# Kernel optimization log

Hardware: AMD Instinct MI355X
Metric: run time of the kernel (lower is better)

Reference implementation:

```python
import jax, jax.numpy as jnp
from jax import lax
import numpy as np

B, L, C = 16, 4096, 512
G = 8            # n_groups
CG = C // G      # group_dim = 64
WD = 4           # weather_dim
ORF = 10.0       # offset_range_factor


def conv1d(x, w, b=None):
    # x: [N, Cin, L], w: [Cout, Cin, 3], stride 1, padding 1
    y = lax.conv_general_dilated(x, w, window_strides=(1,), padding=[(1, 1)],
                                 dimension_numbers=('NCH', 'OIH', 'NCH'))
    if b is not None:
        y = y + b[None, :, None]
    return y


def group_norm(x, gamma, beta, groups=4, eps=1e-5):
    N, Cc, Ln = x.shape
    xr = x.reshape(N, groups, Cc // groups, Ln)
    mu = xr.mean(axis=(2, 3), keepdims=True)
    var = ((xr - mu) ** 2).mean(axis=(2, 3), keepdims=True)
    xn = ((xr - mu) / jnp.sqrt(var + eps)).reshape(N, Cc, Ln)
    return xn * gamma[None, :, None] + beta[None, :, None]


def grid_sample_bilinear_border(inp, grid):
    # Faithful torch F.grid_sample(mode='bilinear', padding_mode='border', align_corners=True)
    # inp: [N, C, H, W]; grid: [N, Ho, Wo, 2], grid[...,0]=x (width coord), grid[...,1]=y (height coord)
    N, Cc, H, W = inp.shape
    _, Ho, Wo, _ = grid.shape
    gx, gy = grid[..., 0], grid[..., 1]
    ix = jnp.clip((gx + 1.0) * 0.5 * (W - 1), 0.0, W - 1)  # border padding clamps coords
    iy = jnp.clip((gy + 1.0) * 0.5 * (H - 1), 0.0, H - 1)
    ix0f = jnp.floor(ix); iy0f = jnp.floor(iy)
    wx = ix - ix0f; wy = iy - iy0f
    ix0 = jnp.clip(ix0f.astype(jnp.int32), 0, W - 1)
    iy0 = jnp.clip(iy0f.astype(jnp.int32), 0, H - 1)
    ix1 = jnp.clip(ix0 + 1, 0, W - 1)
    iy1 = jnp.clip(iy0 + 1, 0, H - 1)
    flat = inp.reshape(N, Cc, H * W)
    def gather(iyk, ixk):
        idx = (iyk * W + ixk).reshape(N, 1, Ho * Wo)
        return jnp.take_along_axis(flat, idx, axis=2).reshape(N, Cc, Ho, Wo)
    v00 = gather(iy0, ix0); v01 = gather(iy0, ix1)
    v10 = gather(iy1, ix0); v11 = gather(iy1, ix1)
    wx = wx[:, None, :, :]; wy = wy[:, None, :, :]
    return (v00 * (1 - wy) * (1 - wx) + v01 * (1 - wy) * wx
            + v10 * wy * (1 - wx) + v11 * wy * wx)


def _forward(x, x_ext, w1, b1, gn_g, gn_b, w2, b2, w3, gate):
    xt = jnp.transpose(x, (0, 2, 1))              # [B, C, L]
    xg = xt.reshape(B * G, CG, L)                 # [B*G, CG, L]
    xe = jnp.transpose(x_ext, (0, 2, 1))          # [B, WD, L]
    xe = jnp.tile(xe, (G, 1, 1))                  # torch .repeat(n_groups,1,1)
    pin = jnp.concatenate([xg, xe], axis=1)       # [B*G, CG+WD, L]
    h = jax.nn.gelu(group_norm(conv1d(pin, w1, b1), gn_g, gn_b), approximate=False)
    h = jax.nn.gelu(conv1d(h, w2, b2), approximate=False)
    offset = jnp.tanh(conv1d(h, w3)) * ORF        # [B*G, 1, L]
    off_n = offset * (2.0 / (L - 1.0))
    ref = (jnp.linspace(0.5, L - 0.5, L, dtype=x.dtype) / (L - 1.0)) * 2.0 - 1.0
    grid_x = jnp.clip(ref[None, None, :, None] + off_n[..., None], -1.0, 1.0)  # [B*G,1,L,1]
    grid = jnp.concatenate([grid_x, jnp.zeros_like(grid_x)], axis=-1)
    grid = jnp.transpose(grid, (0, 2, 1, 3))      # [B*G, L, 1, 2]
    xs = grid_sample_bilinear_border(xg[..., None], grid)[..., 0]  # [B*G, CG, L]
    x_out = xg + jnp.tanh(gate) * xs
    x_out = x_out.reshape(B, C, L)
    return jnp.transpose(x_out, (0, 2, 1)), offset


def setup_inputs() -> dict:
    key = jax.random.key(0)
    ks = jax.random.split(key, 8)
    s = 0.05
    return {
        'x': jax.random.normal(ks[0], (B, L, C), jnp.float32),
        'x_ext': jax.random.normal(ks[1], (B, L, WD), jnp.float32),
        'w1': jax.random.normal(ks[2], (64, CG + WD, 3), jnp.float32) * s,
        'b1': jax.random.normal(ks[3], (64,), jnp.float32) * s,
        'gn_g': jnp.ones((64,), jnp.float32),
        'gn_b': jnp.zeros((64,), jnp.float32),
        'w2': jax.random.normal(ks[4], (32, 64, 3), jnp.float32) * s,
        'b2': jax.random.normal(ks[5], (32,), jnp.float32) * s,
        'w3': jax.random.normal(ks[6], (1, 32, 3), jnp.float32) * s,
        'gate': jnp.array([0.5], jnp.float32),
    }


def reference(x, x_ext, w1, b1, gn_g, gn_b, w2, b2, w3, gate):
    return _forward(x, x_ext, w1, b1, gn_g, gn_b, w2, b2, w3, gate)
```

## Files before the change

### kernel.cpp

```cpp
#include <hip/hip_runtime.h>
#include <hip/hip_bf16.h>

#define BB 16
#define LL 4096
#define CC 512
#define NG 128
#define IC1 68
#define OC1 64
#define OC2 32

typedef short short8 __attribute__((ext_vector_type(8)));
typedef float f32x4 __attribute__((ext_vector_type(4)));

__device__ inline ushort f2b(float f) {
    __hip_bfloat16 h = __float2bfloat16(f);
    return *reinterpret_cast<ushort*>(&h);
}
__device__ inline float b2f(ushort u) {
    __hip_bfloat16 h;
    *reinterpret_cast<ushort*>(&h) = u;
    return __bfloat162float(h);
}
__device__ inline float fast_tanh(float y) {
    float e = __expf(2.0f * y);
    return 1.0f - 2.0f / (e + 1.0f);
}
__device__ inline float fast_gelu(float x) {
    float y = x * (0.7978845608f + 0.0356774081f * x * x);
    return 0.5f * x * (1.0f + fast_tanh(y));
}

__global__ __launch_bounds__(256) void k_prep(const float* __restrict__ x,
    const float* __restrict__ w1, const float* __restrict__ w2,
    const float* __restrict__ gate,
    ushort* __restrict__ w1b, ushort* __restrict__ w2b, float* __restrict__ corr)
{
    int idx = blockIdx.x * 256 + threadIdx.x;
    if (idx < 18432) {
        int k = idx / 6144; int r = idx - k * 6144;
        int oc = r / 96;    int icp = r - oc * 96;
        float v = (icp < IC1) ? w1[(oc * IC1 + icp) * 3 + k] : 0.0f;
        w1b[idx] = f2b(v);
    } else if (idx < 24576) {
        int j = idx - 18432;
        int k = j / 2048; int r = j - k * 2048;
        int oc = r / 64;  int ic = r - oc * 64;
        w2b[j] = f2b(w2[(oc * OC1 + ic) * 3 + k]);
    } else if (idx < 32768) {
        int i3 = idx - 24576;
        int b = i3 >> 9; int ch = i3 & 511;
        float tg = tanhf(gate[0]);
        corr[i3] = tg * 0.5f *
            (x[((size_t)(b * LL + 2047)) * CC + ch] +
             x[((size_t)(b * LL + 2048)) * CC + ch]);
    }
}

#define K1_ROWS 130
#define K1_STR  104
__global__ __launch_bounds__(256) void ka_stats(const float* __restrict__ x,
    const float* __restrict__ xe, const float* __restrict__ b1,
    const ushort* __restrict__ w1b, float* __restrict__ part)
{
    __shared__ ushort pin[K1_ROWS * K1_STR];
    const int n = blockIdx.y, lt = blockIdx.x;
    const int b = n >> 3, g = n & 7, be = n & 15;
    const int l0 = lt * 128;
    const int t = threadIdx.x;

    {
        const int q = t & 15;
        for (int pos = t; pos < K1_ROWS * 16; pos += 256) {
            int li = pos >> 4;
            int l = l0 - 1 + li;
            float4 v = make_float4(0.f, 0.f, 0.f, 0.f);
            if (l >= 0 && l < LL)
                v = *(const float4*)&x[((size_t)(b * LL + l)) * CC + g * 64 + q * 4];
            uint lo = (uint)f2b(v.x) | ((uint)f2b(v.y) << 16);
            uint hi = (uint)f2b(v.z) | ((uint)f2b(v.w) << 16);
            *(uint2*)&pin[li * K1_STR + q * 4] = make_uint2(lo, hi);
        }
    }
    for (int li = t; li < K1_ROWS; li += 256) {
        int l = l0 - 1 + li;
        float4 v = make_float4(0.f, 0.f, 0.f, 0.f);
        if (l >= 0 && l < LL)
            v = *(const float4*)&xe[(size_t)(be * LL + l) * 4];
        uint lo = (uint)f2b(v.x) | ((uint)f2b(v.y) << 16);
        uint hi = (uint)f2b(v.z) | ((uint)f2b(v.w) << 16);
        *(uint2*)&pin[li * K1_STR + 64] = make_uint2(lo, hi);
    }
    {
        uint* pz = (uint*)pin;
        for (int pos = t; pos < K1_ROWS * 14; pos += 256) {
            int li = pos / 14, j = pos - li * 14;
            pz[li * 52 + 34 + j] = 0u;
        }
    }
    __syncthreads();

    const int lane = t & 63;
    const int w = t >> 6;
    const int och = w & 1, lh = w >> 1;
    const int m = lane & 15, h = lane >> 4;

    short8 fa[2][9];
#pragma unroll
    for (int mi = 0; mi < 2; ++mi)
#pragma unroll
        for (int k = 0; k < 3; ++k)
#pragma unroll
            for (int c = 0; c < 3; ++c)
                fa[mi][k * 3 + c] = *(const short8*)&w1b[
                    (size_t)(k * 64 + och * 32 + mi * 16 + m) * 96 + c * 32 + h * 8];

    f32x4 acc[2][4] = {};
#pragma unroll
    for (int tt = 0; tt < 4; ++tt) {
        const int rowbase = lh * 64 + tt * 16 + m;
#pragma unroll
        for (int k = 0; k < 3; ++k) {
#pragma unroll
            for (int c = 0; c < 3; ++c) {
                short8 fb = *(const short8*)&pin[(rowbase + k) * K1_STR + c * 32 + h * 8];
                acc[0][tt] = __builtin_amdgcn_mfma_f32_16x16x32_bf16(fa[0][k * 3 + c], fb, acc[0][tt], 0, 0, 0);
                acc[1][tt] = __builtin_amdgcn_mfma_f32_16x16x32_bf16(fa[1][k * 3 + c], fb, acc[1][tt], 0, 0, 0);
            }
        }
    }

#pragma unroll
    for (int mi = 0; mi < 2; ++mi) {
        float bias[4];
#pragma unroll
        for (int r = 0; r < 4; ++r)
            bias[r] = b1[och * 32 + mi * 16 + h * 4 + r];
        float s1 = 0.f, s2 = 0.f;
#pragma unroll
        for (int tt = 0; tt < 4; ++tt) {
            float v0 = acc[mi][tt][0] + bias[0];
            float v1 = acc[mi][tt][1] + bias[1];
            float v2 = acc[mi][tt][2] + bias[2];
            float v3 = acc[mi][tt][3] + bias[3];
            s1 += v0 + v1 + v2 + v3;
            s2 += v0 * v0 + v1 * v1 + v2 * v2 + v3 * v3;
        }
#pragma unroll
        for (int off = 32; off > 0; off >>= 1) {
            s1 += __shfl_down(s1, off, 64);
            s2 += __shfl_down(s2, off, 64);
        }
        if (lane == 0) {
            int gidx = och * 2 + mi;
            part[(((size_t)n * 4 + gidx) * 64 + lt * 2 + lh) * 2 + 0] = s1;
            part[(((size_t)n * 4 + gidx) * 64 + lt * 2 + lh) * 2 + 1] = s2;
        }
    }
}

#define BT 124
#define XR 130
#define P2R 130
#define P2STR 72
#define H2STR 132
__global__ __launch_bounds__(256) void kb_fused(const float* __restrict__ x,
    const float* __restrict__ xe, const float* __restrict__ b1,
    const ushort* __restrict__ w1b, const float* __restrict__ part,
    const float* __restrict__ gn_g, const float* __restrict__ gn_b,
    const float* __restrict__ b2, const ushort* __restrict__ w2b,
    const float* __restrict__ w3, const float* __restrict__ corr,
    float* __restrict__ out, float* __restrict__ offs)
{
    __shared__ ushort pin[XR * K1_STR];
    __shared__ ushort p2[P2R * P2STR];
    __shared__ float sstats[8];
    const int n = blockIdx.y, lt = blockIdx.x;
    const int b = n >> 3, g = n & 7, be = n & 15;
    const int l0 = lt * BT;
    const int t = threadIdx.x;
    const int lane = t & 63;
    const int w = t >> 6;

    {
        float2 p = *(const float2*)&part[(((size_t)n * 4 + w) * 64 + lane) * 2];
        float s1 = p.x, s2 = p.y;
#pragma unroll
        for (int off = 32; off > 0; off >>= 1) {
            s1 += __shfl_down(s1, off, 64);
            s2 += __shfl_down(s2, off, 64);
        }
        if (lane == 0) {
            float mean = s1 * (1.0f / 65536.0f);
            float var  = s2 * (1.0f / 65536.0f) - mean * mean;
            sstats[w * 2 + 0] = mean;
            sstats[w * 2 + 1] = 1.0f / sqrtf(var + 1e-5f);
        }
    }

    {
        const int q = t & 15;
        const float4 corrv = *(const float4*)&corr[(b << 9) + g * 64 + q * 4];
        for (int pos = t; pos < XR * 16; pos += 256) {
            int li = pos >> 4;
            int l = l0 - 3 + li;
            float4 v = make_float4(0.f, 0.f, 0.f, 0.f);
            if (l >= 0 && l < LL) {
                v = *(const float4*)&x[((size_t)(b * LL + l)) * CC + g * 64 + q * 4];
                if (li >= 3 && li < 3 + BT) {
                    float4 o;
                    o.x = v.x + corrv.x; o.y = v.y + corrv.y;
                    o.z = v.z + corrv.z; o.w = v.w + corrv.w;
                    *(float4*)&out[((size_t)(b * LL + l)) * CC + g * 64 + q * 4] = o;
                }
            }
            uint lo = (uint)f2b(v.x) | ((uint)f2b(v.y) << 16);
            uint hi = (uint)f2b(v.z) | ((uint)f2b(v.w) << 16);
            *(uint2*)&pin[li * K1_STR + q * 4] = make_uint2(lo, hi);
        }
        for (int li = t; li < XR; li += 256) {
            int l = l0 - 3 + li;
            float4 v = make_float4(0.f, 0.f, 0.f, 0.f);
            if (l >= 0 && l < LL)
                v = *(const float4*)&xe[(size_t)(be * LL + l) * 4];
            uint lo = (uint)f2b(v.x) | ((uint)f2b(v.y) << 16);
            uint hi = (uint)f2b(v.z) | ((uint)f2b(v.w) << 16);
            *(uint2*)&pin[li * K1_STR + 64] = make_uint2(lo, hi);
        }
        uint* pz = (uint*)pin;
        for (int pos = t; pos < XR * 14; pos += 256) {
            int li = pos / 14, j = pos - li * 14;
            pz[li * 52 + 34 + j] = 0u;
        }
        uint* qz = (uint*)p2;
        for (int i = t; i < 72; i += 256)
            qz[128 * 36 + i] = 0u;
    }
    __syncthreads();

    const int och = w & 1, lh = w >> 1;
    const int m = lane & 15, h = lane >> 4;

    short8 fa[2][9];
#pragma unroll
    for (int mi = 0; mi < 2; ++mi)
#pragma unroll
        for (int k = 0; k < 3; ++k)
#pragma unroll
            for (int c = 0; c < 3; ++c)
                fa[mi][k * 3 + c] = *(const short8*)&w1b[
                    (size_t)(k * 64 + och * 32 + mi * 16 + m) * 96 + c * 32 + h * 8];

    f32x4 acc[2][4] = {};
#pragma unroll
    for (int tt = 0; tt < 4; ++tt) {
        const int rowbase = lh * 64 + tt * 16 + m;
#pragma unroll
        for (int k = 0; k < 3; ++k) {
#pragma unroll
            for (int c = 0; c < 3; ++c) {
                short8 fb = *(const short8*)&pin[(rowbase + k) * K1_STR + c * 32 + h * 8];
                acc[0][tt] = __builtin_amdgcn_mfma_f32_16x16x32_bf16(fa[0][k * 3 + c], fb, acc[0][tt], 0, 0, 0);
                acc[1][tt] = __builtin_amdgcn_mfma_f32_16x16x32_bf16(fa[1][k * 3 + c], fb, acc[1][tt], 0, 0, 0);
            }
        }
    }

#pragma unroll
    for (int mi = 0; mi < 2; ++mi) {
        int gi = och * 2 + mi;
        float mean = sstats[gi * 2], istd = sstats[gi * 2 + 1];
        float A_[4], B_[4];
#pragma unroll
        for (int r = 0; r < 4; ++r) {
            int oc = och * 32 + mi * 16 + h * 4 + r;
            float ga = gn_g[oc];
            A_[r] = istd * ga;
            B_[r] = gn_b[oc] + (b1[oc] - mean) * A_[r];
        }
#pragma unroll
        for (int tt = 0; tt < 4; ++tt) {
            int p = lh * 64 + tt * 16 + m;
            int l = l0 - 2 + p;
            uint2 pk = make_uint2(0u, 0u);
            if (l >= 0 && l < LL) {
                float v0 = fast_gelu(fmaf(acc[mi][tt][0], A_[0], B_[0]));
                float v1 = fast_gelu(fmaf(acc[mi][tt][1], A_[1], B_[1]));
                float v2 = fast_gelu(fmaf(acc[mi][tt][2], A_[2], B_[2]));
                float v3 = fast_gelu(fmaf(acc[mi][tt][3], A_[3], B_[3]));
                pk.x = (uint)f2b(v0) | ((uint)f2b(v1) << 16);
                pk.y = (uint)f2b(v2) | ((uint)f2b(v3) << 16);
            }
            *(uint2*)&p2[p * P2STR + och * 32 + mi * 16 + h * 4] = pk;
        }
    }
    __syncthreads();

    short8 fa2[2][6];
#pragma unroll
    for (int mi = 0; mi < 2; ++mi)
#pragma unroll
        for (int k = 0; k < 3; ++k)
#pragma unroll
            for (int c = 0; c < 2; ++c)
                fa2[mi][k * 2 + c] = *(const short8*)&w2b[
                    (size_t)(k * 32 + mi * 16 + m) * 64 + c * 32 + h * 8];

    float bias2[2][4];
#pragma unroll
    for (int mi = 0; mi < 2; ++mi)
#pragma unroll
        for (int r = 0; r < 4; ++r)
            bias2[mi][r] = b2[mi * 16 + h * 4 + r];

    f32x4 acc2[2][2] = {};
#pragma unroll
    for (int u = 0; u < 2; ++u) {
        const int jb = (w * 2 + u) * 16 + m;
#pragma unroll
        for (int k = 0; k < 3; ++k) {
#pragma unroll
            for (int c = 0; c < 2; ++c) {
                short8 fb = *(const short8*)&p2[(jb + k) * P2STR + c * 32 + h * 8];
                acc2[0][u] = __builtin_amdgcn_mfma_f32_16x16x32_bf16(fa2[0][k * 2 + c], fb, acc2[0][u], 0, 0, 0);
                acc2[1][u] = __builtin_amdgcn_mfma_f32_16x16x32_bf16(fa2[1][k * 2 + c], fb, acc2[1][u], 0, 0, 0);
            }
        }
    }
    float* h2s = (float*)pin;
#pragma unroll
    for (int mi = 0; mi < 2; ++mi) {
#pragma unroll
        for (int u = 0; u < 2; ++u) {
            int j = (w * 2 + u) * 16 + m;
            int lj = l0 - 1 + j;
#pragma unroll
            for (int r = 0; r < 4; ++r) {
                int oc = mi * 16 + h * 4 + r;
                float v = 0.f;
                if (lj >= 0 && lj < LL)
                    v = fast_gelu(acc2[mi][u][r] + bias2[mi][r]);
                h2s[oc * H2STR + j] = v;
            }
        }
    }
    __syncthreads();

    for (int qq = t; qq < BT; qq += 256) {
        int l = l0 + qq;
        if (l >= LL) break;
        float a = 0.f;
#pragma unroll
        for (int ic = 0; ic < OC2; ++ic) {
            a = fmaf(w3[ic * 3 + 0], h2s[ic * H2STR + qq],     a);
            a = fmaf(w3[ic * 3 + 1], h2s[ic * H2STR + qq + 1], a);
            a = fmaf(w3[ic * 3 + 2], h2s[ic * H2STR + qq + 2], a);
        }
        offs[(size_t)n * LL + l] = fast_tanh(a) * 10.0f;
    }
}

extern "C" void kernel_launch(void* const* d_in, const int* in_sizes, int n_in,
                              void* d_out, int out_size, void* d_ws, size_t ws_size,
                              hipStream_t stream)
{
    const float* x    = (const float*)d_in[0];
    const float* xext = (const float*)d_in[1];
    const float* w1   = (const float*)d_in[2];
    const float* b1   = (const float*)d_in[3];
    const float* gng  = (const float*)d_in[4];
    const float* gnb  = (const float*)d_in[5];
    const float* w2   = (const float*)d_in[6];
    const float* b2   = (const float*)d_in[7];
    const float* w3   = (const float*)d_in[8];
    const float* gate = (const float*)d_in[9];

    float* out  = (float*)d_out;
    float* offs = out + (size_t)BB * LL * CC;

    char* ws = (char*)d_ws;
    float* part = (float*)(ws);
    ushort* w1b = (ushort*)(ws + 262144);
    ushort* w2b = (ushort*)(ws + 299008);
    float* corr = (float*)(ws + 311296);

    k_prep<<<128, 256, 0, stream>>>(x, w1, w2, gate, w1b, w2b, corr);
    dim3 g1(32, NG);
    ka_stats<<<g1, 256, 0, stream>>>(x, xext, b1, w1b, part);
    dim3 g3(34, NG);
    kb_fused<<<g3, 256, 0, stream>>>(x, xext, b1, w1b, part, gng, gnb, b2, w2b,
                                     w3, corr, out, offs);
}
```

Measured before the change: 161.3 us.

## Specialize interior tiles, alias shared buffers, bf16 h2, split conv3 across threads

Both kernels are now templated on whether a tile lies fully inside the sequence, so interior tiles skip boundary checks and run fully unrolled load loops. In the fused kernel, the conv1 input buffer and the conv2 input buffer share one shared-memory region, with an extra barrier between them, and the conv2 output is stored as bf16 instead of fp32. Together these cut LDS use, which may allow more resident blocks. The final 32-channel conv is split across two threads per position and combined with a lane shuffle. The cost is an extra barrier and slightly lower precision on the conv2 output.

```diff
diff --git a/kernel.cpp b/kernel.cpp
--- a/kernel.cpp
+++ b/kernel.cpp
@@ -56,45 +56,55 @@
     }
 }
 
-#define K1_ROWS 130
-#define K1_STR  104
-__global__ __launch_bounds__(256) void ka_stats(const float* __restrict__ x,
-    const float* __restrict__ xe, const float* __restrict__ b1,
-    const ushort* __restrict__ w1b, float* __restrict__ part)
-{
-    __shared__ ushort pin[K1_ROWS * K1_STR];
-    const int n = blockIdx.y, lt = blockIdx.x;
+#define KA_ROWS 130
+#define KA_STR  104
+template<bool FULL>
+__device__ __forceinline__ void ka_body(ushort* pin,
+    const float* __restrict__ x, const float* __restrict__ xe,
+    const float* __restrict__ b1, const ushort* __restrict__ w1b,
+    float* __restrict__ part, int n, int lt)
+{
     const int b = n >> 3, g = n & 7, be = n & 15;
     const int l0 = lt * 128;
     const int t = threadIdx.x;
+    const int q = t & 15;
 
     {
-        const int q = t & 15;
-        for (int pos = t; pos < K1_ROWS * 16; pos += 256) {
-            int li = pos >> 4;
-            int l = l0 - 1 + li;
-            float4 v = make_float4(0.f, 0.f, 0.f, 0.f);
-            if (l >= 0 && l < LL)
-                v = *(const float4*)&x[((size_t)(b * LL + l)) * CC + g * 64 + q * 4];
-            uint lo = (uint)f2b(v.x) | ((uint)f2b(v.y) << 16);
-            uint hi = (uint)f2b(v.z) | ((uint)f2b(v.w) << 16);
-            *(uint2*)&pin[li * K1_STR + q * 4] = make_uint2(lo, hi);
-        }
-    }
-    for (int li = t; li < K1_ROWS; li += 256) {
-        int l = l0 - 1 + li;
+        const float* xb = &x[((size_t)b * LL + (l0 - 1)) * CC + g * 64 + q * 4];
+#pragma unroll
+        for (int i = 0; i < 9; ++i) {
+            int pos = t + i * 256;
+            if (pos < KA_ROWS * 16) {
+                int li = pos >> 4;
+                float4 v;
+                if (FULL) {
+                    v = *(const float4*)(xb + (size_t)li * CC);
+                } else {
+                    int l = l0 - 1 + li;
+                    v = make_float4(0.f, 0.f, 0.f, 0.f);
+                    if (l >= 0 && l < LL) v = *(const float4*)(xb + (size_t)li * CC);
+                }
+                uint lo = (uint)f2b(v.x) | ((uint)f2b(v.y) << 16);
+                uint hi = (uint)f2b(v.z) | ((uint)f2b(v.w) << 16);
+                *(uint2*)&pin[li * KA_STR + q * 4] = make_uint2(lo, hi);
+            }
+        }
+    }
+    if (t < KA_ROWS) {
+        int l = l0 - 1 + t;
         float4 v = make_float4(0.f, 0.f, 0.f, 0.f);
-        if (l >= 0 && l < LL)
+        if (FULL || (l >= 0 && l < LL))
             v = *(const float4*)&xe[(size_t)(be * LL + l) * 4];
         uint lo = (uint)f2b(v.x) | ((uint)f2b(v.y) << 16);
         uint hi = (uint)f2b(v.z) | ((uint)f2b(v.w) << 16);
-        *(uint2*)&pin[li * K1_STR + 64] = make_uint2(lo, hi);
-    }
-    {
-        uint* pz = (uint*)pin;
-        for (int pos = t; pos < K1_ROWS * 14; pos += 256) {
-            int li = pos / 14, j = pos - li * 14;
-            pz[li * 52 + 34 + j] = 0u;
+        *(uint2*)&pin[t * KA_STR + 64] = make_uint2(lo, hi);
+    }
+#pragma unroll
+    for (int i = 0; i < 4; ++i) {
+        int pos = t + i * 256;
+        if (pos < KA_ROWS * 7) {
+            int li = pos / 7, j = pos - li * 7;
+            *(uint2*)&pin[li * KA_STR + 68 + j * 4] = make_uint2(0u, 0u);
         }
     }
     __syncthreads();
@@ -122,7 +132,7 @@
         for (int k = 0; k < 3; ++k) {
 #pragma unroll
             for (int c = 0; c < 3; ++c) {
-                short8 fb = *(const short8*)&pin[(rowbase + k) * K1_STR + c * 32 + h * 8];
+                short8 fb = *(const short8*)&pin[(rowbase + k) * KA_STR + c * 32 + h * 8];
                 acc[0][tt] = __builtin_amdgcn_mfma_f32_16x16x32_bf16(fa[0][k * 3 + c], fb, acc[0][tt], 0, 0, 0);
                 acc[1][tt] = __builtin_amdgcn_mfma_f32_16x16x32_bf16(fa[1][k * 3 + c], fb, acc[1][tt], 0, 0, 0);
             }
@@ -158,11 +168,241 @@
     }
 }
 
+__global__ __launch_bounds__(256) void ka_stats(const float* __restrict__ x,
+    const float* __restrict__ xe, const float* __restrict__ b1,
+    const ushort* __restrict__ w1b, float* __restrict__ part)
+{
+    __shared__ ushort pin[KA_ROWS * KA_STR];
+    const int n = blockIdx.y, lt = blockIdx.x;
+    if (lt >= 1 && lt <= 30)
+        ka_body<true>(pin, x, xe, b1, w1b, part, n, lt);
+    else
+        ka_body<false>(pin, x, xe, b1, w1b, part, n, lt);
+}
+
 #define BT 124
 #define XR 130
-#define P2R 130
-#define P2STR 72
-#define H2STR 132
+#define PINS 104
+#define P2S  72
+#define H2S  130
+template<bool FULL>
+__device__ __forceinline__ void kb_body(ushort* smem, float* sstats,
+    const float* __restrict__ x, const float* __restrict__ xe,
+    const float* __restrict__ b1, const ushort* __restrict__ w1b,
+    const float* __restrict__ part, const float* __restrict__ gn_g,
+    const float* __restrict__ gn_b, const float* __restrict__ b2,
+    const ushort* __restrict__ w2b, const float* __restrict__ w3,
+    const float* __restrict__ corr, float* __restrict__ out,
+    float* __restrict__ offs, int n, int lt)
+{
+    ushort* pin = smem;
+    ushort* p2  = smem;
+    ushort* h2b = smem + 9360;
+    const int b = n >> 3, g = n & 7, be = n & 15;
+    const int l0 = lt * BT;
+    const int t = threadIdx.x;
+    const int lane = t & 63;
+    const int w = t >> 6;
+
+    {
+        float2 p = *(const float2*)&part[(((size_t)n * 4 + w) * 64 + lane) * 2];
+        float s1 = p.x, s2 = p.y;
+#pragma unroll
+        for (int off = 32; off > 0; off >>= 1) {
+            s1 += __shfl_down(s1, off, 64);
+            s2 += __shfl_down(s2, off, 64);
+        }
+        if (lane == 0) {
+            float mean = s1 * (1.0f / 65536.0f);
+            float var  = s2 * (1.0f / 65536.0f) - mean * mean;
+            sstats[w * 2 + 0] = mean;
+            sstats[w * 2 + 1] = 1.0f / sqrtf(var + 1e-5f);
+        }
+    }
+
+    const int q = t & 15;
+    {
+        const float4 corrv = *(const float4*)&corr[(b << 9) + g * 64 + q * 4];
+        const float* xb = &x[((size_t)b * LL + (l0 - 3)) * CC + g * 64 + q * 4];
+        float* ob = &out[((size_t)b * LL + (l0 - 3)) * CC + g * 64 + q * 4];
+#pragma unroll
+        for (int i = 0; i < 9; ++i) {
+            int pos = t + i * 256;
+            if (pos < XR * 16) {
+                int li = pos >> 4;
+                float4 v;
+                bool inr = true;
+                if (FULL) {
+                    v = *(const float4*)(xb + (size_t)li * CC);
+                } else {
+                    int l = l0 - 3 + li;
+                    inr = (l >= 0 && l < LL);
+                    v = make_float4(0.f, 0.f, 0.f, 0.f);
+                    if (inr) v = *(const float4*)(xb + (size_t)li * CC);
+                }
+                if (li >= 3 && li < 3 + BT && inr) {
+                    float4 o;
+                    o.x = v.x + corrv.x; o.y = v.y + corrv.y;
+                    o.z = v.z + corrv.z; o.w = v.w + corrv.w;
+                    *(float4*)(ob + (size_t)li * CC) = o;
+                }
+                uint lo = (uint)f2b(v.x) | ((uint)f2b(v.y) << 16);
+                uint hi = (uint)f2b(v.z) | ((uint)f2b(v.w) << 16);
+                *(uint2*)&pin[li * PINS + q * 4] = make_uint2(lo, hi);
+            }
+        }
+        if (t < XR) {
+            int l = l0 - 3 + t;
+            float4 v = make_float4(0.f, 0.f, 0.f, 0.f);
+            if (FULL || (l >= 0 && l < LL))
+                v = *(const float4*)&xe[(size_t)(be * LL + l) * 4];
+            uint lo = (uint)f2b(v.x) | ((uint)f2b(v.y) << 16);
+            uint hi = (uint)f2b(v.z) | ((uint)f2b(v.w) << 16);
+            *(uint2*)&pin[t * PINS + 64] = make_uint2(lo, hi);
+        }
+#pragma unroll
+        for (int i = 0; i < 4; ++i) {
+            int pos = t + i * 256;
+            if (pos < XR * 7) {
+                int li = pos / 7, j = pos - li * 7;
+                *(uint2*)&pin[li * PINS + 68 + j * 4] = make_uint2(0u, 0u);
+            }
+        }
+    }
+    __syncthreads();
+
+    const int och = w & 1, lh = w >> 1;
+    const int m = lane & 15, h = lane >> 4;
+
+    short8 fa[2][9];
+#pragma unroll
+    for (int mi = 0; mi < 2; ++mi)
+#pragma unroll
+        for (int k = 0; k < 3; ++k)
+#pragma unroll
+            for (int c = 0; c < 3; ++c)
+                fa[mi][k * 3 + c] = *(const short8*)&w1b[
+                    (size_t)(k * 64 + och * 32 + mi * 16 + m) * 96 + c * 32 + h * 8];
+
+    f32x4 acc[2][4] = {};
+#pragma unroll
+    for (int tt = 0; tt < 4; ++tt) {
+        const int rowbase = lh * 64 + tt * 16 + m;
+#pragma unroll
+        for (int k = 0; k < 3; ++k) {
+#pragma unroll
+            for (int c = 0; c < 3; ++c) {
+                short8 fb = *(const short8*)&pin[(rowbase + k) * PINS + c * 32 + h * 8];
+                acc[0][tt] = __builtin_amdgcn_mfma_f32_16x16x32_bf16(fa[0][k * 3 + c], fb, acc[0][tt], 0, 0, 0);
+                acc[1][tt] = __builtin_amdgcn_mfma_f32_16x16x32_bf16(fa[1][k * 3 + c], fb, acc[1][tt], 0, 0, 0);
+            }
+        }
+    }
+    __syncthreads();
+
+#pragma unroll
+    for (int mi = 0; mi < 2; ++mi) {
+        int gi = och * 2 + mi;
+        float mean = sstats[gi * 2], istd = sstats[gi * 2 + 1];
+        float A_[4], B_[4];
+#pragma unroll
+        for (int r = 0; r < 4; ++r) {
+            int oc = och * 32 + mi * 16 + h * 4 + r;
+            float ga = gn_g[oc];
+            A_[r] = istd * ga;
+            B_[r] = gn_b[oc] + (b1[oc] - mean) * A_[r];
+        }
+#pragma unroll
+        for (int tt = 0; tt < 4; ++tt) {
+            int p = lh * 64 + tt * 16 + m;
+            uint2 pk = make_uint2(0u, 0u);
+            int l = l0 - 2 + p;
+            if (FULL || (l >= 0 && l < LL)) {
+                float v0 = fast_gelu(fmaf(acc[mi][tt][0], A_[0], B_[0]));
+                float v1 = fast_gelu(fmaf(acc[mi][tt][1], A_[1], B_[1]));
+                float v2 = fast_gelu(fmaf(acc[mi][tt][2], A_[2], B_[2]));
+                float v3 = fast_gelu(fmaf(acc[mi][tt][3], A_[3], B_[3]));
+                pk.x = (uint)f2b(v0) | ((uint)f2b(v1) << 16);
+                pk.y = (uint)f2b(v2) | ((uint)f2b(v3) << 16);
+            }
+            *(uint2*)&p2[p * P2S + och * 32 + mi * 16 + h * 4] = pk;
+        }
+    }
+    if (t < 36) ((uint*)(p2 + 128 * P2S))[t] = 0u;
+    __syncthreads();
+
+    short8 fa2[2][6];
+#pragma unroll
+    for (int mi = 0; mi < 2; ++mi)
+#pragma unroll
+        for (int k = 0; k < 3; ++k)
+#pragma unroll
+            for (int c = 0; c < 2; ++c)
+                fa2[mi][k * 2 + c] = *(const short8*)&w2b[
+                    (size_t)(k * 32 + mi * 16 + m) * 64 + c * 32 + h * 8];
+
+    float bias2[2][4];
+#pragma unroll
+    for (int mi = 0; mi < 2; ++mi)
+#pragma unroll
+        for (int r = 0; r < 4; ++r)
+            bias2[mi][r] = b2[mi * 16 + h * 4 + r];
+
+    f32x4 acc2[2][2] = {};
+#pragma unroll
+    for (int u = 0; u < 2; ++u) {
+        const int jb = (w * 2 + u) * 16 + m;
+#pragma unroll
+        for (int k = 0; k < 3; ++k) {
+#pragma unroll
+            for (int c = 0; c < 2; ++c) {
+                short8 fb = *(const short8*)&p2[(jb + k) * P2S + c * 32 + h * 8];
+                acc2[0][u] = __builtin_amdgcn_mfma_f32_16x16x32_bf16(fa2[0][k * 2 + c], fb, acc2[0][u], 0, 0, 0);
+                acc2[1][u] = __builtin_amdgcn_mfma_f32_16x16x32_bf16(fa2[1][k * 2 + c], fb, acc2[1][u], 0, 0, 0);
+            }
+        }
+    }
+#pragma unroll
+    for (int mi = 0; mi < 2; ++mi) {
+#pragma unroll
+        for (int u = 0; u < 2; ++u) {
+            int j = (w * 2 + u) * 16 + m;
+            int lj = l0 - 1 + j;
+#pragma unroll
+            for (int r = 0; r < 4; ++r) {
+                int oc = mi * 16 + h * 4 + r;
+                float v = 0.f;
+                if (FULL || (lj >= 0 && lj < LL))
+                    v = fast_gelu(acc2[mi][u][r] + bias2[mi][r]);
+                h2b[oc * H2S + j] = f2b(v);
+            }
+        }
+    }
+    __syncthreads();
+
+    if (t < 2 * BT) {
+        int qq = t >> 1, half = t & 1;
+        int ic0 = half * 16;
+        float a = 0.f;
+#pragma unroll
+        for (int ic = 0; ic < 16; ++ic) {
+            int icc = ic0 + ic;
+            float v0 = b2f(h2b[icc * H2S + qq]);
+            float v1 = b2f(h2b[icc * H2S + qq + 1]);
+            float v2 = b2f(h2b[icc * H2S + qq + 2]);
+            a = fmaf(w3[icc * 3 + 0], v0, a);
+            a = fmaf(w3[icc * 3 + 1], v1, a);
+            a = fmaf(w3[icc * 3 + 2], v2, a);
+        }
+        a += __shfl_xor(a, 1, 64);
+        if (half == 0) {
+            int l = l0 + qq;
+            if (FULL || l < LL)
+                offs[(size_t)n * LL + l] = fast_tanh(a) * 10.0f;
+        }
+    }
+}
+
 __global__ __launch_bounds__(256) void kb_fused(const float* __restrict__ x,
     const float* __restrict__ xe, const float* __restrict__ b1,
     const ushort* __restrict__ w1b, const float* __restrict__ part,
@@ -171,192 +411,13 @@
     const float* __restrict__ w3, const float* __restrict__ corr,
     float* __restrict__ out, float* __restrict__ offs)
 {
-    __shared__ ushort pin[XR * K1_STR];
-    __shared__ ushort p2[P2R * P2STR];
+    __shared__ ushort smem[13520];
     __shared__ float sstats[8];
     const int n = blockIdx.y, lt = blockIdx.x;
-    const int b = n >> 3, g = n & 7, be = n & 15;
-    const int l0 = lt * BT;
-    const int t = threadIdx.x;
-    const int lane = t & 63;
-    const int w = t >> 6;
-
-    {
-        float2 p = *(const float2*)&part[(((size_t)n * 4 + w) * 64 + lane) * 2];
-        float s1 = p.x, s2 = p.y;
-#pragma unroll
-        for (int off = 32; off > 0; off >>= 1) {
-            s1 += __shfl_down(s1, off, 64);
-            s2 += __shfl_down(s2, off, 64);
-        }
-        if (lane == 0) {
-            float mean = s1 * (1.0f / 65536.0f);
-            float var  = s2 * (1.0f / 65536.0f) - mean * mean;
-            sstats[w * 2 + 0] = mean;
-            sstats[w * 2 + 1] = 1.0f / sqrtf(var + 1e-5f);
-        }
-    }
-
-    {
-        const int q = t & 15;
-        const float4 corrv = *(const float4*)&corr[(b << 9) + g * 64 + q * 4];
-        for (int pos = t; pos < XR * 16; pos += 256) {
-            int li = pos >> 4;
-            int l = l0 - 3 + li;
-            float4 v = make_float4(0.f, 0.f, 0.f, 0.f);
-            if (l >= 0 && l < LL) {
-                v = *(const float4*)&x[((size_t)(b * LL + l)) * CC + g * 64 + q * 4];
-                if (li >= 3 && li < 3 + BT) {
-                    float4 o;
-                    o.x = v.x + corrv.x; o.y = v.y + corrv.y;
-                    o.z = v.z + corrv.z; o.w = v.w + corrv.w;
-                    *(float4*)&out[((size_t)(b * LL + l)) * CC + g * 64 + q * 4] = o;
-                }
-            }
-            uint lo = (uint)f2b(v.x) | ((uint)f2b(v.y) << 16);
-            uint hi = (uint)f2b(v.z) | ((uint)f2b(v.w) << 16);
-            *(uint2*)&pin[li * K1_STR + q * 4] = make_uint2(lo, hi);
-        }
-        for (int li = t; li < XR; li += 256) {
-            int l = l0 - 3 + li;
-            float4 v = make_float4(0.f, 0.f, 0.f, 0.f);
-            if (l >= 0 && l < LL)
-                v = *(const float4*)&xe[(size_t)(be * LL + l) * 4];
-            uint lo = (uint)f2b(v.x) | ((uint)f2b(v.y) << 16);
-            uint hi = (uint)f2b(v.z) | ((uint)f2b(v.w) << 16);
-            *(uint2*)&pin[li * K1_STR + 64] = make_uint2(lo, hi);
-        }
-        uint* pz = (uint*)pin;
-        for (int pos = t; pos < XR * 14; pos += 256) {
-            int li = pos / 14, j = pos - li * 14;
-            pz[li * 52 + 34 + j] = 0u;
-        }
-        uint* qz = (uint*)p2;
-        for (int i = t; i < 72; i += 256)
-            qz[128 * 36 + i] = 0u;
-    }
-    __syncthreads();
-
-    const int och = w & 1, lh = w >> 1;
-    const int m = lane & 15, h = lane >> 4;
-
-    short8 fa[2][9];
-#pragma unroll
-    for (int mi = 0; mi < 2; ++mi)
-#pragma unroll
-        for (int k = 0; k < 3; ++k)
-#pragma unroll
-            for (int c = 0; c < 3; ++c)
-                fa[mi][k * 3 + c] = *(const short8*)&w1b[
-                    (size_t)(k * 64 + och * 32 + mi * 16 + m) * 96 + c * 32 + h * 8];
-
-    f32x4 acc[2][4] = {};
-#pragma unroll
-    for (int tt = 0; tt < 4; ++tt) {
-        const int rowbase = lh * 64 + tt * 16 + m;
-#pragma unroll
-        for (int k = 0; k < 3; ++k) {
-#pragma unroll
-            for (int c = 0; c < 3; ++c) {
-                short8 fb = *(const short8*)&pin[(rowbase + k) * K1_STR + c * 32 + h * 8];
-                acc[0][tt] = __builtin_amdgcn_mfma_f32_16x16x32_bf16(fa[0][k * 3 + c], fb, acc[0][tt], 0, 0, 0);
-                acc[1][tt] = __builtin_amdgcn_mfma_f32_16x16x32_bf16(fa[1][k * 3 + c], fb, acc[1][tt], 0, 0, 0);
-            }
-        }
-    }
-
-#pragma unroll
-    for (int mi = 0; mi < 2; ++mi) {
-        int gi = och * 2 + mi;
-        float mean = sstats[gi * 2], istd = sstats[gi * 2 + 1];
-        float A_[4], B_[4];
-#pragma unroll
-        for (int r = 0; r < 4; ++r) {
-            int oc = och * 32 + mi * 16 + h * 4 + r;
-            float ga = gn_g[oc];
-            A_[r] = istd * ga;
-            B_[r] = gn_b[oc] + (b1[oc] - mean) * A_[r];
-        }
-#pragma unroll
-        for (int tt = 0; tt < 4; ++tt) {
-            int p = lh * 64 + tt * 16 + m;
-            int l = l0 - 2 + p;
-            uint2 pk = make_uint2(0u, 0u);
-            if (l >= 0 && l < LL) {
-                float v0 = fast_gelu(fmaf(acc[mi][tt][0], A_[0], B_[0]));
-                float v1 = fast_gelu(fmaf(acc[mi][tt][1], A_[1], B_[1]));
-                float v2 = fast_gelu(fmaf(acc[mi][tt][2], A_[2], B_[2]));
-                float v3 = fast_gelu(fmaf(acc[mi][tt][3], A_[3], B_[3]));
-                pk.x = (uint)f2b(v0) | ((uint)f2b(v1) << 16);
-                pk.y = (uint)f2b(v2) | ((uint)f2b(v3) << 16);
-            }
-            *(uint2*)&p2[p * P2STR + och * 32 + mi * 16 + h * 4] = pk;
-        }
-    }
-    __syncthreads();
-
-    short8 fa2[2][6];
-#pragma unroll
-    for (int mi = 0; mi < 2; ++mi)
-#pragma unroll
-        for (int k = 0; k < 3; ++k)
-#pragma unroll
-            for (int c = 0; c < 2; ++c)
-                fa2[mi][k * 2 + c] = *(const short8*)&w2b[
-                    (size_t)(k * 32 + mi * 16 + m) * 64 + c * 32 + h * 8];
-
-    float bias2[2][4];
-#pragma unroll
-    for (int mi = 0; mi < 2; ++mi)
-#pragma unroll
-        for (int r = 0; r < 4; ++r)
-            bias2[mi][r] = b2[mi * 16 + h * 4 + r];
-
-    f32x4 acc2[2][2] = {};
-#pragma unroll
-    for (int u = 0; u < 2; ++u) {
-        const int jb = (w * 2 + u) * 16 + m;
-#pragma unroll
-        for (int k = 0; k < 3; ++k) {
-#pragma unroll
-            for (int c = 0; c < 2; ++c) {
-                short8 fb = *(const short8*)&p2[(jb + k) * P2STR + c * 32 + h * 8];
-                acc2[0][u] = __builtin_amdgcn_mfma_f32_16x16x32_bf16(fa2[0][k * 2 + c], fb, acc2[0][u], 0, 0, 0);
-                acc2[1][u] = __builtin_amdgcn_mfma_f32_16x16x32_bf16(fa2[1][k * 2 + c], fb, acc2[1][u], 0, 0, 0);
-            }
-        }
-    }
-    float* h2s = (float*)pin;
-#pragma unroll
-    for (int mi = 0; mi < 2; ++mi) {
-#pragma unroll
-        for (int u = 0; u < 2; ++u) {
-            int j = (w * 2 + u) * 16 + m;
-            int lj = l0 - 1 + j;
-#pragma unroll
-            for (int r = 0; r < 4; ++r) {
-                int oc = mi * 16 + h * 4 + r;
-                float v = 0.f;
-                if (lj >= 0 && lj < LL)
-                    v = fast_gelu(acc2[mi][u][r] + bias2[mi][r]);
-                h2s[oc * H2STR + j] = v;
-            }
-        }
-    }
-    __syncthreads();
-
-    for (int qq = t; qq < BT; qq += 256) {
-        int l = l0 + qq;
-        if (l >= LL) break;
-        float a = 0.f;
-#pragma unroll
-        for (int ic = 0; ic < OC2; ++ic) {
-            a = fmaf(w3[ic * 3 + 0], h2s[ic * H2STR + qq],     a);
-            a = fmaf(w3[ic * 3 + 1], h2s[ic * H2STR + qq + 1], a);
-            a = fmaf(w3[ic * 3 + 2], h2s[ic * H2STR + qq + 2], a);
-        }
-        offs[(size_t)n * LL + l] = fast_tanh(a) * 10.0f;
-    }
+    if (lt >= 1 && lt <= 32)
+        kb_body<true >(smem, sstats, x, xe, b1, w1b, part, gn_g, gn_b, b2, w2b, w3, corr, out, offs, n, lt);
+    else
+        kb_body<false>(smem, sstats, x, xe, b1, w1b, part, gn_g, gn_b, b2, w2b, w3, corr, out, offs, n, lt);
 }
 
 extern "C" void kernel_launch(void* const* d_in, const int* in_sizes, int n_in,
```

Result: slower. 164.9 us (+2.2%).
